# Optimization experiments

Hardware: AMD Instinct MI355X
Metric: run time of the kernel (lower is better)

Reference implementation:

```python
import jax, jax.numpy as jnp
import numpy as np

N = 50000
NEG_SLOPE = 0.2


def gat_conv(x, src, dst, W, a_src, a_dst, b):
    # PyG GATConv, heads=1: h = xW; e_ij = LeakyReLU(a_src.h_j + a_dst.h_i);
    # softmax over edges sharing destination i; out_i = sum_j alpha_ij h_j + b.
    h = x @ W                                   # [N, F]
    as_ = h @ a_src                             # [N]
    ad_ = h @ a_dst                             # [N]
    e = jax.nn.leaky_relu(as_[src] + ad_[dst], NEG_SLOPE)  # [E]
    m = jax.ops.segment_max(e, dst, num_segments=N)        # per-dst max
    m = jnp.where(jnp.isfinite(m), m, 0.0)
    p = jnp.exp(e - m[dst])
    denom = jax.ops.segment_sum(p, dst, num_segments=N)
    alpha = p / jnp.maximum(denom[dst], 1e-16)             # [E]
    out = jax.ops.segment_sum(alpha[:, None] * h[src], dst, num_segments=N)
    return out + b


def setup_inputs() -> dict:
    key = jax.random.key(0)
    ks = jax.random.split(key, 12)
    E, L = 800000, 262144
    F_in, F_mid, F_out = 128, 64, 32
    x = jax.random.normal(ks[0], (N, F_in), dtype=jnp.float32)
    edge_index = jax.random.randint(ks[1], (2, E), 0, N, dtype=jnp.int32)
    edge_label_index = jax.random.randint(ks[2], (2, L), 0, N, dtype=jnp.int32)
    s1 = 1.0 / np.sqrt(F_in)
    s2 = 1.0 / np.sqrt(F_mid)
    return {
        "x": x,
        "edge_index": edge_index,
        "edge_label_index": edge_label_index,
        "W1": jax.random.normal(ks[3], (F_in, F_mid), jnp.float32) * s1,
        "a_src1": jax.random.normal(ks[4], (F_mid,), jnp.float32) * s2,
        "a_dst1": jax.random.normal(ks[5], (F_mid,), jnp.float32) * s2,
        "b1": jnp.zeros((F_mid,), jnp.float32),
        "W2": jax.random.normal(ks[6], (F_mid, F_out), jnp.float32) * s2,
        "a_src2": jax.random.normal(ks[7], (F_out,), jnp.float32) * (1.0 / np.sqrt(F_out)),
        "a_dst2": jax.random.normal(ks[8], (F_out,), jnp.float32) * (1.0 / np.sqrt(F_out)),
        "b2": jnp.zeros((F_out,), jnp.float32),
    }


def reference(x, edge_index, edge_label_index, W1, a_src1, a_dst1, b1, W2, a_src2, a_dst2, b2):
    # add self-loops (PyG GATConv default add_self_loops=True)
    loops = jnp.arange(N, dtype=edge_index.dtype)
    src = jnp.concatenate([edge_index[0], loops])
    dst = jnp.concatenate([edge_index[1], loops])
    z = jax.nn.relu(gat_conv(x, src, dst, W1, a_src1, a_dst1, b1))
    z = gat_conv(z, src, dst, W2, a_src2, a_dst2, b2)
    # dot-product decode over candidate edges
    return jnp.sum(z[edge_label_index[0]] * z[edge_label_index[1]], axis=-1)
```

## Files before the change

### kernel.cpp

```cpp
#include <hip/hip_runtime.h>

#define NN 50000
#define NEG 0.2f
#define NBUCK 196
#define NBLK 208

__device__ __forceinline__ float leaky(float v) { return v > 0.0f ? v : NEG * v; }

__device__ __forceinline__ unsigned f2bf(float x) {
    unsigned u = __float_as_uint(x);
    return (u + 0x7FFFu + ((u >> 16) & 1u)) >> 16;
}
__device__ __forceinline__ float bf2f(unsigned short u) {
    return __uint_as_float(((unsigned)u) << 16);
}

__global__ __launch_bounds__(256) void k_hist_gemm1(
        const int* __restrict__ ei, int E, int T, int CHUNK,
        int* __restrict__ bh,
        const float* __restrict__ x, const float* __restrict__ W,
        const float* __restrict__ a_src, const float* __restrict__ a_dst,
        unsigned int* __restrict__ hu, float* __restrict__ as_, float* __restrict__ ad_) {
    __shared__ float xs[4][8][128];
    __shared__ int hist[NBUCK];
    int tid = threadIdx.x;
    if (blockIdx.x < NBLK) {
        if (tid < NBUCK) hist[tid] = 0;
        __syncthreads();
        int beg = blockIdx.x * CHUNK;
        int end = min(beg + CHUNK, T);
        for (int i = beg + tid; i < end; i += 256) {
            int dv = (i < E) ? ei[E + i] : (i - E);
            atomicAdd(&hist[dv >> 8], 1);
        }
        __syncthreads();
        if (tid < NBUCK) bh[blockIdx.x * NBUCK + tid] = hist[tid];
        return;
    }
    int gblock = blockIdx.x - NBLK;
    int wl = tid >> 6;
    int lane = tid & 63;
    int base = (gblock * 4 + wl) * 8;
    if (base >= NN) return;
#pragma unroll
    for (int n = 0; n < 8; ++n) {
        int node = base + n;
        xs[wl][n][lane]      = x[node * 128 + lane];
        xs[wl][n][lane + 64] = x[node * 128 + 64 + lane];
    }
    float acc[8] = {0, 0, 0, 0, 0, 0, 0, 0};
#pragma unroll 8
    for (int kg = 0; kg < 32; ++kg) {
        float w0 = W[(4 * kg + 0) * 64 + lane];
        float w1 = W[(4 * kg + 1) * 64 + lane];
        float w2 = W[(4 * kg + 2) * 64 + lane];
        float w3 = W[(4 * kg + 3) * 64 + lane];
#pragma unroll
        for (int n = 0; n < 8; ++n) {
            float4 xv = *(const float4*)&xs[wl][n][kg * 4];
            acc[n] = fmaf(xv.x, w0, fmaf(xv.y, w1, fmaf(xv.z, w2, fmaf(xv.w, w3, acc[n]))));
        }
    }
    float pa = a_src[lane], pd = a_dst[lane];
#pragma unroll
    for (int n = 0; n < 8; ++n) {
        int node = base + n;
        unsigned my = f2bf(acc[n]);
        unsigned nb = __shfl_down(my, 1, 64);
        if ((lane & 1) == 0) hu[node * 32 + (lane >> 1)] = my | (nb << 16);
        float s = acc[n] * pa;
        float d = acc[n] * pd;
#pragma unroll
        for (int off = 32; off > 0; off >>= 1) {
            s += __shfl_xor(s, off, 64);
            d += __shfl_xor(d, off, 64);
        }
        if (lane == 0) { as_[node] = s; ad_[node] = d; }
    }
}

__global__ __launch_bounds__(256) void k_scan_col(int* __restrict__ bh,
                                                  int* __restrict__ btot) {
    int k = blockIdx.x;
    int tid = threadIdx.x;
    __shared__ int wsum[4];
    int v = (tid < NBLK) ? bh[tid * NBUCK + k] : 0;
    int lane = tid & 63, w = tid >> 6;
    int inc = v;
#pragma unroll
    for (int off = 1; off < 64; off <<= 1) {
        int t = __shfl_up(inc, off, 64);
        if (lane >= off) inc += t;
    }
    if (lane == 63) wsum[w] = inc;
    __syncthreads();
    int wpre = 0;
    for (int q = 0; q < w; ++q) wpre += wsum[q];
    int excl = wpre + inc - v;
    if (tid < NBLK) bh[tid * NBUCK + k] = excl;
    if (tid == 255) btot[k] = wpre + inc;
}

__global__ __launch_bounds__(256) void k_part(
        const int* __restrict__ ei, int E, int T, int CHUNK,
        const int* __restrict__ bh, const int* __restrict__ btot,
        unsigned int* __restrict__ part) {
    __shared__ int cur[NBUCK];
    __shared__ int wsum[4];
    int tid = threadIdx.x;
    int v = (tid < NBUCK) ? btot[tid] : 0;
    int lane = tid & 63, w = tid >> 6;
    int inc = v;
#pragma unroll
    for (int off = 1; off < 64; off <<= 1) {
        int t = __shfl_up(inc, off, 64);
        if (lane >= off) inc += t;
    }
    if (lane == 63) wsum[w] = inc;
    __syncthreads();
    int wpre = 0;
    for (int q = 0; q < w; ++q) wpre += wsum[q];
    if (tid < NBUCK) cur[tid] = (wpre + inc - v) + bh[blockIdx.x * NBUCK + tid];
    __syncthreads();
    int beg = blockIdx.x * CHUNK;
    int end = min(beg + CHUNK, T);
    for (int i = beg + tid; i < end; i += 256) {
        int sv, dv;
        if (i < E) { sv = ei[i]; dv = ei[E + i]; }
        else { sv = dv = i - E; }
        int pos = atomicAdd(&cur[dv >> 8], 1);
        part[pos] = (unsigned)sv | ((unsigned)(dv & 255) << 16);
    }
}

__global__ __launch_bounds__(256) void k_csr(
        const unsigned int* __restrict__ part, const int* __restrict__ btot,
        int2* __restrict__ rc, unsigned short* __restrict__ csr_src) {
    int k = blockIdx.x;
    int tid = threadIdx.x;
    __shared__ int hist[256], roff[256], wsum[4];
    int lane = tid & 63, w = tid >> 6;
    {
        int v = (tid < k) ? btot[tid] : 0;
#pragma unroll
        for (int off = 32; off > 0; off >>= 1) v += __shfl_xor(v, off, 64);
        if (lane == 0) wsum[w] = v;
    }
    hist[tid] = 0;
    __syncthreads();
    int beg = wsum[0] + wsum[1] + wsum[2] + wsum[3];
    int end = beg + btot[k];
    for (int i = beg + tid; i < end; i += 256)
        atomicAdd(&hist[part[i] >> 16], 1);
    __syncthreads();
    int v = hist[tid];
    int inc = v;
#pragma unroll
    for (int off = 1; off < 64; off <<= 1) {
        int t = __shfl_up(inc, off, 64);
        if (lane >= off) inc += t;
    }
    __syncthreads();
    if (lane == 63) wsum[w] = inc;
    __syncthreads();
    int wpre = 0;
    for (int q = 0; q < w; ++q) wpre += wsum[q];
    int excl = wpre + inc - v;
    roff[tid] = beg + excl;
    int dst = (k << 8) + tid;
    if (dst < NN) rc[dst] = make_int2(beg + excl, v);
    __syncthreads();
    for (int i = beg + tid; i < end; i += 256) {
        unsigned int e = part[i];
        int pos = atomicAdd(&roff[e >> 16], 1);
        csr_src[pos] = (unsigned short)(e & 0xFFFFu);
    }
}

__global__ void k_aggr1(const int2* __restrict__ rc,
                        const unsigned short* __restrict__ csr_src,
                        const float* __restrict__ as_, const float* __restrict__ ad_,
                        const unsigned int* __restrict__ hu, const float* __restrict__ b,
                        float* __restrict__ out) {
    int gid = blockIdx.x * blockDim.x + threadIdx.x;
    int dst = gid >> 5;
    int f = gid & 31;
    if (dst >= NN) return;
    int2 rcv = rc[dst];
    int start = rcv.x;
    int deg = rcv.y;
    float ad = ad_[dst];
    float ssum, ax = 0.0f, ay = 0.0f;

    if (deg <= 32) {
        int sj = 0;
        float ej = -1e30f;
        if (f < deg) {
            sj = csr_src[start + f];
            ej = leaky(as_[sj] + ad);
        }
        float m = ej;
#pragma unroll
        for (int off = 16; off > 0; off >>= 1) m = fmaxf(m, __shfl_xor(m, off, 32));
        float pj = (f < deg) ? __expf(ej - m) : 0.0f;
        ssum = pj;
#pragma unroll
        for (int off = 16; off > 0; off >>= 1) ssum += __shfl_xor(ssum, off, 32);
        int t = 0;
        for (; t + 4 <= deg; t += 4) {
            int s0 = __shfl(sj, t, 32), s1 = __shfl(sj, t + 1, 32);
            int s2 = __shfl(sj, t + 2, 32), s3 = __shfl(sj, t + 3, 32);
            float p0 = __shfl(pj, t, 32), p1 = __shfl(pj, t + 1, 32);
            float p2 = __shfl(pj, t + 2, 32), p3 = __shfl(pj, t + 3, 32);
            unsigned g0 = hu[s0 * 32 + f];
            unsigned g1 = hu[s1 * 32 + f];
            unsigned g2 = hu[s2 * 32 + f];
            unsigned g3 = hu[s3 * 32 + f];
            ax = fmaf(p0, __uint_as_float(g0 << 16), ax);
            ay = fmaf(p0, __uint_as_float(g0 & 0xFFFF0000u), ay);
            ax = fmaf(p1, __uint_as_float(g1 << 16), ax);
            ay = fmaf(p1, __uint_as_float(g1 & 0xFFFF0000u), ay);
            ax = fmaf(p2, __uint_as_float(g2 << 16), ax);
            ay = fmaf(p2, __uint_as_float(g2 & 0xFFFF0000u), ay);
            ax = fmaf(p3, __uint_as_float(g3 << 16), ax);
            ay = fmaf(p3, __uint_as_float(g3 & 0xFFFF0000u), ay);
        }
        for (; t < deg; ++t) {
            int sv = __shfl(sj, t, 32);
            float pv = __shfl(pj, t, 32);
            unsigned g = hu[sv * 32 + f];
            ax = fmaf(pv, __uint_as_float(g << 16), ax);
            ay = fmaf(pv, __uint_as_float(g & 0xFFFF0000u), ay);
        }
    } else {
        float m = -1e30f;
        for (int base = 0; base < deg; base += 32) {
            int j = base + f;
            if (j < deg) m = fmaxf(m, leaky(as_[csr_src[start + j]] + ad));
        }
#pragma unroll
        for (int off = 16; off > 0; off >>= 1) m = fmaxf(m, __shfl_xor(m, off, 32));
        ssum = 0.0f;
        for (int base = 0; base < deg; base += 32) {
            int j = base + f;
            int sj = 0;
            float pj = 0.0f;
            if (j < deg) {
                sj = csr_src[start + j];
                pj = __expf(leaky(as_[sj] + ad) - m);
            }
            ssum += pj;
            int lim = min(32, deg - base);
            for (int t = 0; t < lim; ++t) {
                int sv = __shfl(sj, t, 32);
                float pv = __shfl(pj, t, 32);
                unsigned g = hu[sv * 32 + f];
                ax = fmaf(pv, __uint_as_float(g << 16), ax);
                ay = fmaf(pv, __uint_as_float(g & 0xFFFF0000u), ay);
            }
        }
#pragma unroll
        for (int off = 16; off > 0; off >>= 1) ssum += __shfl_xor(ssum, off, 32);
    }

    float inv = 1.0f / ssum;
    float2 bb = *(const float2*)&b[2 * f];
    float2 r;
    r.x = fmaxf(ax * inv + bb.x, 0.0f);
    r.y = fmaxf(ay * inv + bb.y, 0.0f);
    *(float2*)&out[dst * 64 + 2 * f] = r;
}

__global__ __launch_bounds__(256) void k_gemm2(
        const float* __restrict__ z, const float* __restrict__ W,
        const float* __restrict__ a_src, const float* __restrict__ a_dst,
        unsigned int* __restrict__ hu2, float* __restrict__ as_, float* __restrict__ ad_) {
    int wave = (blockIdx.x * blockDim.x + threadIdx.x) >> 6;
    int lane = threadIdx.x & 63;
    int g = lane >> 5;
    int f = lane & 31;
    int wl = threadIdx.x >> 6;
    __shared__ float zs[4][16][64];
    int base = wave * 16;
    if (base >= NN) return;
#pragma unroll
    for (int n = 0; n < 16; ++n) zs[wl][n][lane] = z[(base + n) * 64 + lane];
    float wreg[32];
#pragma unroll
    for (int kk = 0; kk < 32; ++kk) wreg[kk] = W[(g * 32 + kk) * 32 + f];
    float pa = a_src[f], pd = a_dst[f];
#pragma unroll 4
    for (int n = 0; n < 16; ++n) {
        int node = base + n;
        float part = 0.0f;
#pragma unroll
        for (int kg = 0; kg < 8; ++kg) {
            float4 zv = *(const float4*)&zs[wl][n][g * 32 + kg * 4];
            part = fmaf(zv.x, wreg[4 * kg + 0],
                   fmaf(zv.y, wreg[4 * kg + 1],
                   fmaf(zv.z, wreg[4 * kg + 2],
                   fmaf(zv.w, wreg[4 * kg + 3], part))));
        }
        float hv = part + __shfl_xor(part, 32, 64);
        unsigned my = f2bf(hv);
        unsigned nb = __shfl_down(my, 1, 64);
        if (g == 0 && (f & 1) == 0) hu2[node * 16 + (f >> 1)] = my | (nb << 16);
        float s = hv * pa, d = hv * pd;
#pragma unroll
        for (int off = 16; off > 0; off >>= 1) {
            s += __shfl_xor(s, off, 64);
            d += __shfl_xor(d, off, 64);
        }
        if (lane == 0) { as_[node] = s; ad_[node] = d; }
    }
}

__global__ void k_aggr2(const int2* __restrict__ rc,
                        const unsigned short* __restrict__ csr_src,
                        const float* __restrict__ as_, const float* __restrict__ ad_,
                        const unsigned short* __restrict__ h2u, const float* __restrict__ b,
                        float* __restrict__ out) {
    const int F = 32;
    int gid = blockIdx.x * blockDim.x + threadIdx.x;
    int dst = gid / F;
    int f = gid % F;
    if (dst >= NN) return;
    int2 rcv = rc[dst];
    int start = rcv.x;
    int deg = rcv.y;
    float ad = ad_[dst];
    float ssum, acc = 0.0f;

    if (deg <= F) {
        int sj = 0;
        float ej = -1e30f;
        if (f < deg) {
            sj = csr_src[start + f];
            ej = leaky(as_[sj] + ad);
        }
        float m = ej;
#pragma unroll
        for (int off = F / 2; off > 0; off >>= 1) m = fmaxf(m, __shfl_xor(m, off, F));
        float pj = (f < deg) ? __expf(ej - m) : 0.0f;
        ssum = pj;
#pragma unroll
        for (int off = F / 2; off > 0; off >>= 1) ssum += __shfl_xor(ssum, off, F);
        int t = 0;
        for (; t + 4 <= deg; t += 4) {
            int s0 = __shfl(sj, t, F), s1 = __shfl(sj, t + 1, F);
            int s2 = __shfl(sj, t + 2, F), s3 = __shfl(sj, t + 3, F);
            float p0 = __shfl(pj, t, F), p1 = __shfl(pj, t + 1, F);
            float p2 = __shfl(pj, t + 2, F), p3 = __shfl(pj, t + 3, F);
            float g0 = bf2f(h2u[s0 * F + f]);
            float g1 = bf2f(h2u[s1 * F + f]);
            float g2 = bf2f(h2u[s2 * F + f]);
            float g3 = bf2f(h2u[s3 * F + f]);
            acc = fmaf(p0, g0, acc);
            acc = fmaf(p1, g1, acc);
            acc = fmaf(p2, g2, acc);
            acc = fmaf(p3, g3, acc);
        }
        for (; t < deg; ++t) {
            int sv = __shfl(sj, t, F);
            float pv = __shfl(pj, t, F);
            acc = fmaf(pv, bf2f(h2u[sv * F + f]), acc);
        }
    } else {
        float m = -1e30f;
        for (int base = 0; base < deg; base += F) {
            int j = base + f;
            if (j < deg) m = fmaxf(m, leaky(as_[csr_src[start + j]] + ad));
        }
#pragma unroll
        for (int off = F / 2; off > 0; off >>= 1) m = fmaxf(m, __shfl_xor(m, off, F));
        ssum = 0.0f;
        for (int base = 0; base < deg; base += F) {
            int j = base + f;
            int sj = 0;
            float pj = 0.0f;
            if (j < deg) {
                sj = csr_src[start + j];
                pj = __expf(leaky(as_[sj] + ad) - m);
            }
            ssum += pj;
            int lim = min(F, deg - base);
            for (int t = 0; t < lim; ++t) {
                int sv = __shfl(sj, t, F);
                float pv = __shfl(pj, t, F);
                acc = fmaf(pv, bf2f(h2u[sv * F + f]), acc);
            }
        }
#pragma unroll
        for (int off = F / 2; off > 0; off >>= 1) ssum += __shfl_xor(ssum, off, F);
    }

    out[dst * F + f] = acc / ssum + b[f];
}

__global__ void k_decode(const int* __restrict__ eli, int L,
                         const float* __restrict__ z2, float* __restrict__ out) {
    int gid = blockIdx.x * blockDim.x + threadIdx.x;
    int pair = gid >> 3;
    int f4 = gid & 7;
    if (pair >= L) return;
    int i = eli[pair];
    int j = eli[L + pair];
    float4 a = *(const float4*)&z2[i * 32 + f4 * 4];
    float4 b = *(const float4*)&z2[j * 32 + f4 * 4];
    float v = a.x * b.x + a.y * b.y + a.z * b.z + a.w * b.w;
#pragma unroll
    for (int off = 4; off > 0; off >>= 1) v += __shfl_xor(v, off, 8);
    if (f4 == 0) out[pair] = v;
}

extern "C" void kernel_launch(void* const* d_in, const int* in_sizes, int n_in,
                              void* d_out, int out_size, void* d_ws, size_t ws_size,
                              hipStream_t stream) {
    const float* x     = (const float*)d_in[0];
    const int*   ei    = (const int*)d_in[1];
    const int*   eli   = (const int*)d_in[2];
    const float* W1    = (const float*)d_in[3];
    const float* asrc1 = (const float*)d_in[4];
    const float* adst1 = (const float*)d_in[5];
    const float* b1    = (const float*)d_in[6];
    const float* W2    = (const float*)d_in[7];
    const float* asrc2 = (const float*)d_in[8];
    const float* adst2 = (const float*)d_in[9];
    const float* b2    = (const float*)d_in[10];
    float* out = (float*)d_out;

    const int E = in_sizes[1] / 2;
    const int L = in_sizes[2] / 2;
    const int T = E + NN;
    const int CHUNK = (T + NBLK - 1) / NBLK;

    float* ws  = (float*)d_ws;
    unsigned int* hu  = (unsigned int*)ws;
    unsigned int* hu2 = hu + NN * 32;
    float* z1  = (float*)(hu2 + NN * 16);
    float* z2  = z1 + NN * 64;
    float* as1 = z2 + NN * 32;
    float* ad1 = as1 + NN;
    float* as2 = ad1 + NN;
    float* ad2 = as2 + NN;
    int2* rc         = (int2*)(ad2 + NN);
    int* btot        = (int*)(rc + NN);
    int* bh          = btot + NBUCK;
    unsigned int*   part    = (unsigned int*)(bh + NBLK * NBUCK);
    unsigned short* csr_src = (unsigned short*)(part + T);

    const int GB = (NN / 8 + 3) / 4;

    k_hist_gemm1<<<NBLK + GB, 256, 0, stream>>>(ei, E, T, CHUNK, bh,
                                                x, W1, asrc1, adst1, hu, as1, ad1);
    k_scan_col<<<NBUCK, 256, 0, stream>>>(bh, btot);
    k_part<<<NBLK, 256, 0, stream>>>(ei, E, T, CHUNK, bh, btot, part);
    k_csr<<<NBUCK, 256, 0, stream>>>(part, btot, rc, csr_src);

    k_aggr1<<<(NN * 32 + 255) / 256, 256, 0, stream>>>(
        rc, csr_src, as1, ad1, hu, b1, z1);

    k_gemm2<<<(NN / 16 + 3) / 4, 256, 0, stream>>>(z1, W2, asrc2, adst2, hu2, as2, ad2);
    k_aggr2<<<(NN * 32 + 255) / 256, 256, 0, stream>>>(
        rc, csr_src, as2, ad2, (const unsigned short*)hu2, b2, z2);

    k_decode<<<(L * 8 + 255) / 256, 256, 0, stream>>>(eli, L, z2, out);
}
```

Measured before the change: 219.2 us.

## Fuse layer-1 aggregation with layer-2 GEMM and halve lanes per node

```diff
diff --git a/kernel.cpp b/kernel.cpp
--- a/kernel.cpp
+++ b/kernel.cpp
@@ -11,9 +11,8 @@
     unsigned u = __float_as_uint(x);
     return (u + 0x7FFFu + ((u >> 16) & 1u)) >> 16;
 }
-__device__ __forceinline__ float bf2f(unsigned short u) {
-    return __uint_as_float(((unsigned)u) << 16);
-}
+__device__ __forceinline__ float bflo(unsigned g) { return __uint_as_float(g << 16); }
+__device__ __forceinline__ float bfhi(unsigned g) { return __uint_as_float(g & 0xFFFF0000u); }
 
 __global__ __launch_bounds__(256) void k_hist_gemm1(
         const int* __restrict__ ei, int E, int T, int CHUNK,
@@ -177,71 +176,83 @@
     }
 }
 
-__global__ void k_aggr1(const int2* __restrict__ rc,
-                        const unsigned short* __restrict__ csr_src,
-                        const float* __restrict__ as_, const float* __restrict__ ad_,
-                        const unsigned int* __restrict__ hu, const float* __restrict__ b,
-                        float* __restrict__ out) {
-    int gid = blockIdx.x * blockDim.x + threadIdx.x;
-    int dst = gid >> 5;
-    int f = gid & 31;
-    if (dst >= NN) return;
+__global__ __launch_bounds__(256) void k_aggr1g2(
+        const int2* __restrict__ rc, const unsigned short* __restrict__ csr_src,
+        const float* __restrict__ as_, const float* __restrict__ ad_,
+        const unsigned int* __restrict__ hu, const float* __restrict__ b1,
+        const float* __restrict__ W2, const float* __restrict__ a2s,
+        const float* __restrict__ a2d,
+        unsigned int* __restrict__ hu2, float* __restrict__ as2,
+        float* __restrict__ ad2) {
+    __shared__ float w2s[64 * 32];
+    int tid = threadIdx.x;
+#pragma unroll
+    for (int i = 0; i < 8; ++i) w2s[tid + 256 * i] = W2[tid + 256 * i];
+    __syncthreads();
+    int f = tid & 15;
+    int dst = blockIdx.x * 16 + (tid >> 4);
     int2 rcv = rc[dst];
-    int start = rcv.x;
-    int deg = rcv.y;
+    int start = rcv.x, deg = rcv.y;
     float ad = ad_[dst];
-    float ssum, ax = 0.0f, ay = 0.0f;
+    float a0 = 0, a1 = 0, a2 = 0, a3 = 0, ssum;
 
     if (deg <= 32) {
-        int sj = 0;
-        float ej = -1e30f;
-        if (f < deg) {
-            sj = csr_src[start + f];
-            ej = leaky(as_[sj] + ad);
-        }
-        float m = ej;
-#pragma unroll
-        for (int off = 16; off > 0; off >>= 1) m = fmaxf(m, __shfl_xor(m, off, 32));
-        float pj = (f < deg) ? __expf(ej - m) : 0.0f;
-        ssum = pj;
-#pragma unroll
-        for (int off = 16; off > 0; off >>= 1) ssum += __shfl_xor(ssum, off, 32);
+        int nA = min(deg, 16);
+        int sA = 0, sB = 0;
+        float eA = -1e30f, eB = -1e30f;
+        if (f < nA) { sA = csr_src[start + f]; eA = leaky(as_[sA] + ad); }
+        if (16 + f < deg) { sB = csr_src[start + 16 + f]; eB = leaky(as_[sB] + ad); }
+        float m = fmaxf(eA, eB);
+#pragma unroll
+        for (int off = 8; off > 0; off >>= 1) m = fmaxf(m, __shfl_xor(m, off, 16));
+        float pA = (f < nA) ? __expf(eA - m) : 0.0f;
+        float pB = (16 + f < deg) ? __expf(eB - m) : 0.0f;
+        ssum = pA + pB;
+#pragma unroll
+        for (int off = 8; off > 0; off >>= 1) ssum += __shfl_xor(ssum, off, 16);
         int t = 0;
-        for (; t + 4 <= deg; t += 4) {
-            int s0 = __shfl(sj, t, 32), s1 = __shfl(sj, t + 1, 32);
-            int s2 = __shfl(sj, t + 2, 32), s3 = __shfl(sj, t + 3, 32);
-            float p0 = __shfl(pj, t, 32), p1 = __shfl(pj, t + 1, 32);
-            float p2 = __shfl(pj, t + 2, 32), p3 = __shfl(pj, t + 3, 32);
-            unsigned g0 = hu[s0 * 32 + f];
-            unsigned g1 = hu[s1 * 32 + f];
-            unsigned g2 = hu[s2 * 32 + f];
-            unsigned g3 = hu[s3 * 32 + f];
-            ax = fmaf(p0, __uint_as_float(g0 << 16), ax);
-            ay = fmaf(p0, __uint_as_float(g0 & 0xFFFF0000u), ay);
-            ax = fmaf(p1, __uint_as_float(g1 << 16), ax);
-            ay = fmaf(p1, __uint_as_float(g1 & 0xFFFF0000u), ay);
-            ax = fmaf(p2, __uint_as_float(g2 << 16), ax);
-            ay = fmaf(p2, __uint_as_float(g2 & 0xFFFF0000u), ay);
-            ax = fmaf(p3, __uint_as_float(g3 << 16), ax);
-            ay = fmaf(p3, __uint_as_float(g3 & 0xFFFF0000u), ay);
-        }
-        for (; t < deg; ++t) {
-            int sv = __shfl(sj, t, 32);
-            float pv = __shfl(pj, t, 32);
-            unsigned g = hu[sv * 32 + f];
-            ax = fmaf(pv, __uint_as_float(g << 16), ax);
-            ay = fmaf(pv, __uint_as_float(g & 0xFFFF0000u), ay);
+        for (; t + 4 <= nA; t += 4) {
+            int s0 = __shfl(sA, t, 16), s1 = __shfl(sA, t + 1, 16);
+            int s2 = __shfl(sA, t + 2, 16), s3 = __shfl(sA, t + 3, 16);
+            float p0 = __shfl(pA, t, 16), p1 = __shfl(pA, t + 1, 16);
+            float p2 = __shfl(pA, t + 2, 16), p3 = __shfl(pA, t + 3, 16);
+            uint2 g0 = *(const uint2*)&hu[s0 * 32 + 2 * f];
+            uint2 g1 = *(const uint2*)&hu[s1 * 32 + 2 * f];
+            uint2 g2 = *(const uint2*)&hu[s2 * 32 + 2 * f];
+            uint2 g3 = *(const uint2*)&hu[s3 * 32 + 2 * f];
+            a0 = fmaf(p0, bflo(g0.x), a0); a1 = fmaf(p0, bfhi(g0.x), a1);
+            a2 = fmaf(p0, bflo(g0.y), a2); a3 = fmaf(p0, bfhi(g0.y), a3);
+            a0 = fmaf(p1, bflo(g1.x), a0); a1 = fmaf(p1, bfhi(g1.x), a1);
+            a2 = fmaf(p1, bflo(g1.y), a2); a3 = fmaf(p1, bfhi(g1.y), a3);
+            a0 = fmaf(p2, bflo(g2.x), a0); a1 = fmaf(p2, bfhi(g2.x), a1);
+            a2 = fmaf(p2, bflo(g2.y), a2); a3 = fmaf(p2, bfhi(g2.y), a3);
+            a0 = fmaf(p3, bflo(g3.x), a0); a1 = fmaf(p3, bfhi(g3.x), a1);
+            a2 = fmaf(p3, bflo(g3.y), a2); a3 = fmaf(p3, bfhi(g3.y), a3);
+        }
+        for (; t < nA; ++t) {
+            int sv = __shfl(sA, t, 16);
+            float pv = __shfl(pA, t, 16);
+            uint2 g = *(const uint2*)&hu[sv * 32 + 2 * f];
+            a0 = fmaf(pv, bflo(g.x), a0); a1 = fmaf(pv, bfhi(g.x), a1);
+            a2 = fmaf(pv, bflo(g.y), a2); a3 = fmaf(pv, bfhi(g.y), a3);
+        }
+        for (t = 16; t < deg; ++t) {
+            int sv = __shfl(sB, t - 16, 16);
+            float pv = __shfl(pB, t - 16, 16);
+            uint2 g = *(const uint2*)&hu[sv * 32 + 2 * f];
+            a0 = fmaf(pv, bflo(g.x), a0); a1 = fmaf(pv, bfhi(g.x), a1);
+            a2 = fmaf(pv, bflo(g.y), a2); a3 = fmaf(pv, bfhi(g.y), a3);
         }
     } else {
         float m = -1e30f;
-        for (int base = 0; base < deg; base += 32) {
+        for (int base = 0; base < deg; base += 16) {
             int j = base + f;
             if (j < deg) m = fmaxf(m, leaky(as_[csr_src[start + j]] + ad));
         }
 #pragma unroll
-        for (int off = 16; off > 0; off >>= 1) m = fmaxf(m, __shfl_xor(m, off, 32));
+        for (int off = 8; off > 0; off >>= 1) m = fmaxf(m, __shfl_xor(m, off, 16));
         ssum = 0.0f;
-        for (int base = 0; base < deg; base += 32) {
+        for (int base = 0; base < deg; base += 16) {
             int j = base + f;
             int sj = 0;
             float pj = 0.0f;
@@ -250,131 +261,119 @@
                 pj = __expf(leaky(as_[sj] + ad) - m);
             }
             ssum += pj;
-            int lim = min(32, deg - base);
+            int lim = min(16, deg - base);
             for (int t = 0; t < lim; ++t) {
-                int sv = __shfl(sj, t, 32);
-                float pv = __shfl(pj, t, 32);
-                unsigned g = hu[sv * 32 + f];
-                ax = fmaf(pv, __uint_as_float(g << 16), ax);
-                ay = fmaf(pv, __uint_as_float(g & 0xFFFF0000u), ay);
+                int sv = __shfl(sj, t, 16);
+                float pv = __shfl(pj, t, 16);
+                uint2 g = *(const uint2*)&hu[sv * 32 + 2 * f];
+                a0 = fmaf(pv, bflo(g.x), a0); a1 = fmaf(pv, bfhi(g.x), a1);
+                a2 = fmaf(pv, bflo(g.y), a2); a3 = fmaf(pv, bfhi(g.y), a3);
             }
         }
 #pragma unroll
-        for (int off = 16; off > 0; off >>= 1) ssum += __shfl_xor(ssum, off, 32);
+        for (int off = 8; off > 0; off >>= 1) ssum += __shfl_xor(ssum, off, 16);
     }
 
     float inv = 1.0f / ssum;
-    float2 bb = *(const float2*)&b[2 * f];
-    float2 r;
-    r.x = fmaxf(ax * inv + bb.x, 0.0f);
-    r.y = fmaxf(ay * inv + bb.y, 0.0f);
-    *(float2*)&out[dst * 64 + 2 * f] = r;
-}
-
-__global__ __launch_bounds__(256) void k_gemm2(
-        const float* __restrict__ z, const float* __restrict__ W,
-        const float* __restrict__ a_src, const float* __restrict__ a_dst,
-        unsigned int* __restrict__ hu2, float* __restrict__ as_, float* __restrict__ ad_) {
-    int wave = (blockIdx.x * blockDim.x + threadIdx.x) >> 6;
-    int lane = threadIdx.x & 63;
-    int g = lane >> 5;
-    int f = lane & 31;
-    int wl = threadIdx.x >> 6;
-    __shared__ float zs[4][16][64];
-    int base = wave * 16;
-    if (base >= NN) return;
-#pragma unroll
-    for (int n = 0; n < 16; ++n) zs[wl][n][lane] = z[(base + n) * 64 + lane];
-    float wreg[32];
-#pragma unroll
-    for (int kk = 0; kk < 32; ++kk) wreg[kk] = W[(g * 32 + kk) * 32 + f];
-    float pa = a_src[f], pd = a_dst[f];
+    float4 bb = *(const float4*)&b1[4 * f];
+    float z0 = fmaxf(fmaf(a0, inv, bb.x), 0.0f);
+    float z1 = fmaxf(fmaf(a1, inv, bb.y), 0.0f);
+    float z2 = fmaxf(fmaf(a2, inv, bb.z), 0.0f);
+    float z3 = fmaxf(fmaf(a3, inv, bb.w), 0.0f);
+
+    float h0 = 0.0f, h1 = 0.0f;
 #pragma unroll 4
-    for (int n = 0; n < 16; ++n) {
-        int node = base + n;
-        float part = 0.0f;
-#pragma unroll
-        for (int kg = 0; kg < 8; ++kg) {
-            float4 zv = *(const float4*)&zs[wl][n][g * 32 + kg * 4];
-            part = fmaf(zv.x, wreg[4 * kg + 0],
-                   fmaf(zv.y, wreg[4 * kg + 1],
-                   fmaf(zv.z, wreg[4 * kg + 2],
-                   fmaf(zv.w, wreg[4 * kg + 3], part))));
-        }
-        float hv = part + __shfl_xor(part, 32, 64);
-        unsigned my = f2bf(hv);
-        unsigned nb = __shfl_down(my, 1, 64);
-        if (g == 0 && (f & 1) == 0) hu2[node * 16 + (f >> 1)] = my | (nb << 16);
-        float s = hv * pa, d = hv * pd;
-#pragma unroll
-        for (int off = 16; off > 0; off >>= 1) {
-            s += __shfl_xor(s, off, 64);
-            d += __shfl_xor(d, off, 64);
-        }
-        if (lane == 0) { as_[node] = s; ad_[node] = d; }
-    }
+    for (int t = 0; t < 16; ++t) {
+        float y0 = __shfl(z0, t, 16);
+        float y1 = __shfl(z1, t, 16);
+        float y2 = __shfl(z2, t, 16);
+        float y3 = __shfl(z3, t, 16);
+        const float2* wp = (const float2*)&w2s[(4 * t) * 32 + 2 * f];
+        float2 w0v = wp[0];
+        float2 w1v = wp[16];
+        float2 w2v = wp[32];
+        float2 w3v = wp[48];
+        h0 = fmaf(y0, w0v.x, fmaf(y1, w1v.x, fmaf(y2, w2v.x, fmaf(y3, w3v.x, h0))));
+        h1 = fmaf(y0, w0v.y, fmaf(y1, w1v.y, fmaf(y2, w2v.y, fmaf(y3, w3v.y, h1))));
+    }
+    float2 av = *(const float2*)&a2s[2 * f];
+    float2 dv = *(const float2*)&a2d[2 * f];
+    float sa = fmaf(h0, av.x, h1 * av.y);
+    float sd = fmaf(h0, dv.x, h1 * dv.y);
+#pragma unroll
+    for (int off = 8; off > 0; off >>= 1) {
+        sa += __shfl_xor(sa, off, 16);
+        sd += __shfl_xor(sd, off, 16);
+    }
+    if (f == 0) { as2[dst] = sa; ad2[dst] = sd; }
+    hu2[dst * 16 + f] = f2bf(h0) | (f2bf(h1) << 16);
 }
 
 __global__ void k_aggr2(const int2* __restrict__ rc,
                         const unsigned short* __restrict__ csr_src,
                         const float* __restrict__ as_, const float* __restrict__ ad_,
-                        const unsigned short* __restrict__ h2u, const float* __restrict__ b,
+                        const unsigned int* __restrict__ hu2, const float* __restrict__ b,
                         float* __restrict__ out) {
-    const int F = 32;
     int gid = blockIdx.x * blockDim.x + threadIdx.x;
-    int dst = gid / F;
-    int f = gid % F;
+    int dst = gid >> 4;
+    int f = gid & 15;
     if (dst >= NN) return;
     int2 rcv = rc[dst];
-    int start = rcv.x;
-    int deg = rcv.y;
+    int start = rcv.x, deg = rcv.y;
     float ad = ad_[dst];
-    float ssum, acc = 0.0f;
-
-    if (deg <= F) {
-        int sj = 0;
-        float ej = -1e30f;
-        if (f < deg) {
-            sj = csr_src[start + f];
-            ej = leaky(as_[sj] + ad);
-        }
-        float m = ej;
-#pragma unroll
-        for (int off = F / 2; off > 0; off >>= 1) m = fmaxf(m, __shfl_xor(m, off, F));
-        float pj = (f < deg) ? __expf(ej - m) : 0.0f;
-        ssum = pj;
-#pragma unroll
-        for (int off = F / 2; off > 0; off >>= 1) ssum += __shfl_xor(ssum, off, F);
+    float a0 = 0, a1 = 0, ssum;
+
+    if (deg <= 32) {
+        int nA = min(deg, 16);
+        int sA = 0, sB = 0;
+        float eA = -1e30f, eB = -1e30f;
+        if (f < nA) { sA = csr_src[start + f]; eA = leaky(as_[sA] + ad); }
+        if (16 + f < deg) { sB = csr_src[start + 16 + f]; eB = leaky(as_[sB] + ad); }
+        float m = fmaxf(eA, eB);
+#pragma unroll
+        for (int off = 8; off > 0; off >>= 1) m = fmaxf(m, __shfl_xor(m, off, 16));
+        float pA = (f < nA) ? __expf(eA - m) : 0.0f;
+        float pB = (16 + f < deg) ? __expf(eB - m) : 0.0f;
+        ssum = pA + pB;
+#pragma unroll
+        for (int off = 8; off > 0; off >>= 1) ssum += __shfl_xor(ssum, off, 16);
         int t = 0;
-        for (; t + 4 <= deg; t += 4) {
-            int s0 = __shfl(sj, t, F), s1 = __shfl(sj, t + 1, F);
-            int s2 = __shfl(sj, t + 2, F), s3 = __shfl(sj, t + 3, F);
-            float p0 = __shfl(pj, t, F), p1 = __shfl(pj, t + 1, F);
-            float p2 = __shfl(pj, t + 2, F), p3 = __shfl(pj, t + 3, F);
-            float g0 = bf2f(h2u[s0 * F + f]);
-            float g1 = bf2f(h2u[s1 * F + f]);
-            float g2 = bf2f(h2u[s2 * F + f]);
-            float g3 = bf2f(h2u[s3 * F + f]);
-            acc = fmaf(p0, g0, acc);
-            acc = fmaf(p1, g1, acc);
-            acc = fmaf(p2, g2, acc);
-            acc = fmaf(p3, g3, acc);
-        }
-        for (; t < deg; ++t) {
-            int sv = __shfl(sj, t, F);
-            float pv = __shfl(pj, t, F);
-            acc = fmaf(pv, bf2f(h2u[sv * F + f]), acc);
+        for (; t + 4 <= nA; t += 4) {
+            int s0 = __shfl(sA, t, 16), s1 = __shfl(sA, t + 1, 16);
+            int s2 = __shfl(sA, t + 2, 16), s3 = __shfl(sA, t + 3, 16);
+            float p0 = __shfl(pA, t, 16), p1 = __shfl(pA, t + 1, 16);
+            float p2 = __shfl(pA, t + 2, 16), p3 = __shfl(pA, t + 3, 16);
+            unsigned g0 = hu2[s0 * 16 + f];
+            unsigned g1 = hu2[s1 * 16 + f];
+            unsigned g2 = hu2[s2 * 16 + f];
+            unsigned g3 = hu2[s3 * 16 + f];
+            a0 = fmaf(p0, bflo(g0), a0); a1 = fmaf(p0, bfhi(g0), a1);
+            a0 = fmaf(p1, bflo(g1), a0); a1 = fmaf(p1, bfhi(g1), a1);
+            a0 = fmaf(p2, bflo(g2), a0); a1 = fmaf(p2, bfhi(g2), a1);
+            a0 = fmaf(p3, bflo(g3), a0); a1 = fmaf(p3, bfhi(g3), a1);
+        }
+        for (; t < nA; ++t) {
+            int sv = __shfl(sA, t, 16);
+            float pv = __shfl(pA, t, 16);
+            unsigned g = hu2[sv * 16 + f];
+            a0 = fmaf(pv, bflo(g), a0); a1 = fmaf(pv, bfhi(g), a1);
+        }
+        for (t = 16; t < deg; ++t) {
+            int sv = __shfl(sB, t - 16, 16);
+            float pv = __shfl(pB, t - 16, 16);
+            unsigned g = hu2[sv * 16 + f];
+            a0 = fmaf(pv, bflo(g), a0); a1 = fmaf(pv, bfhi(g), a1);
         }
     } else {
         float m = -1e30f;
-        for (int base = 0; base < deg; base += F) {
+        for (int base = 0; base < deg; base += 16) {
             int j = base + f;
             if (j < deg) m = fmaxf(m, leaky(as_[csr_src[start + j]] + ad));
         }
 #pragma unroll
-        for (int off = F / 2; off > 0; off >>= 1) m = fmaxf(m, __shfl_xor(m, off, F));
+        for (int off = 8; off > 0; off >>= 1) m = fmaxf(m, __shfl_xor(m, off, 16));
         ssum = 0.0f;
-        for (int base = 0; base < deg; base += F) {
+        for (int base = 0; base < deg; base += 16) {
             int j = base + f;
             int sj = 0;
             float pj = 0.0f;
@@ -383,18 +382,24 @@
                 pj = __expf(leaky(as_[sj] + ad) - m);
             }
             ssum += pj;
-            int lim = min(F, deg - base);
+            int lim = min(16, deg - base);
             for (int t = 0; t < lim; ++t) {
-                int sv = __shfl(sj, t, F);
-                float pv = __shfl(pj, t, F);
-                acc = fmaf(pv, bf2f(h2u[sv * F + f]), acc);
+                int sv = __shfl(sj, t, 16);
+                float pv = __shfl(pj, t, 16);
+                unsigned g = hu2[sv * 16 + f];
+                a0 = fmaf(pv, bflo(g), a0); a1 = fmaf(pv, bfhi(g), a1);
             }
         }
 #pragma unroll
-        for (int off = F / 2; off > 0; off >>= 1) ssum += __shfl_xor(ssum, off, F);
-    }
-
-    out[dst * F + f] = acc / ssum + b[f];
+        for (int off = 8; off > 0; off >>= 1) ssum += __shfl_xor(ssum, off, 16);
+    }
+
+    float inv = 1.0f / ssum;
+    float2 bb = *(const float2*)&b[2 * f];
+    float2 r;
+    r.x = fmaf(a0, inv, bb.x);
+    r.y = fmaf(a1, inv, bb.y);
+    *(float2*)&out[dst * 32 + 2 * f] = r;
 }
 
 __global__ void k_decode(const int* __restrict__ eli, int L,
@@ -437,8 +442,7 @@
     float* ws  = (float*)d_ws;
     unsigned int* hu  = (unsigned int*)ws;
     unsigned int* hu2 = hu + NN * 32;
-    float* z1  = (float*)(hu2 + NN * 16);
-    float* z2  = z1 + NN * 64;
+    float* z2  = (float*)(hu2 + NN * 16);
     float* as1 = z2 + NN * 32;
     float* ad1 = as1 + NN;
     float* as2 = ad1 + NN;
@@ -457,12 +461,11 @@
     k_part<<<NBLK, 256, 0, stream>>>(ei, E, T, CHUNK, bh, btot, part);
     k_csr<<<NBUCK, 256, 0, stream>>>(part, btot, rc, csr_src);
 
-    k_aggr1<<<(NN * 32 + 255) / 256, 256, 0, stream>>>(
-        rc, csr_src, as1, ad1, hu, b1, z1);
-
-    k_gemm2<<<(NN / 16 + 3) / 4, 256, 0, stream>>>(z1, W2, asrc2, adst2, hu2, as2, ad2);
-    k_aggr2<<<(NN * 32 + 255) / 256, 256, 0, stream>>>(
-        rc, csr_src, as2, ad2, (const unsigned short*)hu2, b2, z2);
+    k_aggr1g2<<<NN / 16, 256, 0, stream>>>(rc, csr_src, as1, ad1, hu, b1,
+                                           W2, asrc2, adst2, hu2, as2, ad2);
+
+    k_aggr2<<<(NN * 16 + 255) / 256, 256, 0, stream>>>(
+        rc, csr_src, as2, ad2, hu2, b2, z2);
 
     k_decode<<<(L * 8 + 255) / 256, 256, 0, stream>>>(eli, L, z2, out);
 }
```

After: 210.6 us. -3.9%, faster.
